# Performance work log

Measured on AMD Instinct MI355X. Metric: run time of the kernel, lower is better.

Reference implementation:

```python
import jax, jax.numpy as jnp
import numpy as np

ROPE_THETA = 10000.0

def _apply_rope(x, theta=ROPE_THETA):
    # x: [B, H, L, d_head]
    L, d_k = x.shape[-2], x.shape[-1]
    inv_freq = 1.0 / (theta ** (jnp.arange(0, d_k, 2, dtype=jnp.float32) / d_k))  # [d_k/2]
    ang = jnp.arange(L, dtype=jnp.float32)[:, None] * inv_freq[None, :]           # [L, d_k/2]
    ang = jnp.repeat(ang, 2, axis=-1)                                             # [L, d_k] interleaved
    xr = x.reshape(x.shape[:-1] + (d_k // 2, 2))
    rot = jnp.stack((-xr[..., 1], xr[..., 0]), axis=-1).reshape(x.shape)
    return x * jnp.cos(ang) + rot * jnp.sin(ang)

def setup_inputs() -> dict:
    key = jax.random.key(0)
    k1, k2, k3 = jax.random.split(key, 3)
    B, L, D = 2, 2048, 2048
    std_qkv = np.sqrt(2.0 / (D + 3 * D)).astype(np.float32)
    std_o = np.sqrt(2.0 / (D + D)).astype(np.float32)
    return {
        "x": jax.random.normal(k1, (B, L, D), dtype=jnp.float32),
        "W_qkv": jax.random.normal(k2, (3 * D, D), dtype=jnp.float32) * std_qkv,
        "W_o": jax.random.normal(k3, (D, D), dtype=jnp.float32) * std_o,
    }

def reference(x, W_qkv, W_o):
    B, L, D = x.shape
    H = 16
    dh = D // H
    qkv = jnp.einsum('bld,ed->ble', x, W_qkv)            # [B, L, 3D]
    q, k, v = jnp.split(qkv, 3, axis=-1)
    # [B, H, L, dh]
    q = q.reshape(B, L, H, dh).transpose(0, 2, 1, 3)
    k = k.reshape(B, L, H, dh).transpose(0, 2, 1, 3)
    v = v.reshape(B, L, H, dh).transpose(0, 2, 1, 3)
    q = _apply_rope(q)
    k = _apply_rope(k)
    scale = 1.0 / np.sqrt(dh).astype(np.float32)
    att = jnp.einsum('bhqd,bhkd->bhqk', q, k) * scale    # [B, H, L, L]
    causal = jnp.tril(jnp.ones((L, L), dtype=bool))
    att = jnp.where(causal, att, -jnp.inf)
    p = jax.nn.softmax(att, axis=-1)
    y = jnp.einsum('bhqk,bhkd->bhqd', p, v)              # [B, H, L, dh]
    y = y.transpose(0, 2, 1, 3).reshape(B, L, D)
    return jnp.einsum('bld,ed->ble', y, W_o)
```

## Files before the change

### kernel.cpp

```cpp
#include <hip/hip_runtime.h>
#include <math.h>

typedef __bf16 bf16x8 __attribute__((ext_vector_type(8)));
typedef float f32x4 __attribute__((ext_vector_type(4)));
typedef unsigned short us8 __attribute__((ext_vector_type(8)));

#define B_ 2
#define L_ 2048
#define D_ 2048
#define H_ 16
#define DH 128

__device__ __forceinline__ unsigned short f2b(float f) {
  union { float f; unsigned u; } v; v.f = f;
  unsigned u = v.u;
  return (unsigned short)((u + 0x7fffu + ((u >> 16) & 1u)) >> 16);
}
__device__ __forceinline__ float b2f(unsigned short h) {
  union { unsigned u; float f; } v; v.u = ((unsigned)h) << 16;
  return v.f;
}

#define GLD16(g, l) __builtin_amdgcn_global_load_lds(                          \
    (const __attribute__((address_space(1))) void*)(g),                        \
    (__attribute__((address_space(3))) void*)(l), 16, 0, 0)

__global__ void f32_to_bf16(const float* __restrict__ in,
                            unsigned short* __restrict__ out, int n4) {
  int i = blockIdx.x * blockDim.x + threadIdx.x;
  const int stride = gridDim.x * blockDim.x;
  for (; i < n4; i += stride) {
    const float4 v = ((const float4*)in)[i];
    ushort4 o;
    o.x = f2b(v.x); o.y = f2b(v.y); o.z = f2b(v.z); o.w = f2b(v.w);
    ((ushort4*)out)[i] = o;
  }
}


#define SB()                              \
  do {                                    \
    __builtin_amdgcn_s_barrier();         \
    __builtin_amdgcn_sched_barrier(0);    \
  } while (0)

#define VMC2() asm volatile("s_waitcnt vmcnt(2)" ::: "memory")

#define LOAD_A(BUF, MH)                                                        \
  _Pragma("unroll") for (int q = 0; q < 4; ++q) {                              \
    const int rowA = (MH) * 64 + q * 16 + lo;                                  \
    _Pragma("unroll") for (int kk = 0; kk < 2; ++kk)                           \
        af[q][kk] = *(const bf16x8*)&lds[0][BUF][wmh]                          \
            [rowA * 64 + ((kk * 4 + hi) ^ sw) * 8];                            \
  }

#define LOAD_B(BUF, NH)                                                        \
  _Pragma("unroll") for (int j = 0; j < 2; ++j) {                              \
    const int rowB = bro + ((NH) * 2 + j) * 16;                                \
    _Pragma("unroll") for (int kk = 0; kk < 2; ++kk)                           \
        bfr[j][kk] = *(const bf16x8*)&lds[1][BUF][bhalf]                       \
            [rowB * 64 + ((kk * 4 + hi) ^ sw) * 8];                            \
  }

#define MFMA16(MH, NH)                                                         \
  do {                                                                         \
    __builtin_amdgcn_s_setprio(1);                                             \
    _Pragma("unroll") for (int q = 0; q < 4; ++q) {                            \
      _Pragma("unroll") for (int j = 0; j < 2; ++j) {                          \
        acc[(MH) * 4 + q][(NH) * 2 + j] =                                      \
            __builtin_amdgcn_mfma_f32_16x16x32_bf16(                           \
                af[q][0], bfr[j][0], acc[(MH) * 4 + q][(NH) * 2 + j], 0, 0, 0);\
        acc[(MH) * 4 + q][(NH) * 2 + j] =                                      \
            __builtin_amdgcn_mfma_f32_16x16x32_bf16(                           \
                af[q][1], bfr[j][1], acc[(MH) * 4 + q][(NH) * 2 + j], 0, 0, 0);\
      }                                                                        \
    }                                                                          \
    __builtin_amdgcn_s_setprio(0);                                             \
  } while (0)

template <bool OUT_BF16>
__global__ __launch_bounds__(512)
void gemm8p(const unsigned short* __restrict__ A,
            const unsigned short* __restrict__ Bm,
            void* __restrict__ Cv, int M, int N, int K) {
  __shared__ __align__(16) unsigned short lds[2][2][2][128 * 64];
  const int tid = threadIdx.x;
  const int w = tid >> 6, lane = tid & 63;
  const int lo = lane & 15, hi = lane >> 4, sw = lo & 7;
  const int wmh = w >> 2;
  const int wn = (w & 3) * 64;
  const int bhalf = wn >> 7, bro = (wn & 64) + lo;
  const int GM = M >> 8;
  const int nwg = gridDim.x;
  const int f = blockIdx.x;
  const int v = (f & 7) * (nwg >> 3) + (f >> 3);
  const int bn = v / GM, bm = v % GM;
  const int NI = K >> 7;

  auto stageU = [&](int mat, int buf, int half, int tile) {
    const unsigned short* G = mat ? Bm : A;
    const int r256 = (mat ? bn : bm) * 256 + half * 128;
#pragma unroll
    for (int u = 0; u < 2; ++u) {
      const int c = u * 512 + tid;
      const int row = c >> 3;
      const int gs = (c & 7) ^ (row & 7);
      GLD16(G + (long)(r256 + row) * K + tile * 64 + gs * 8,
            &lds[mat][buf][half][(u * 512 + (tid & ~63)) * 8]);
    }
  };

  f32x4 acc[8][4] = {};
  bf16x8 af[4][2], bfr[2][2];

  stageU(0, 0, 0, 0); stageU(0, 0, 1, 0);
  stageU(1, 0, 0, 0); stageU(1, 0, 1, 0);
  stageU(0, 1, 0, 1);
  VMC2();
  SB();

  for (int i = 0; i < NI; ++i) {
    const int t1 = 2 * i + 1;
    const bool nx = (i + 1 < NI);
    LOAD_A(0, 0) LOAD_B(0, 0)
    stageU(1, 1, 0, t1);
    SB(); MFMA16(0, 0); SB();
    LOAD_B(0, 1)
    stageU(0, 1, 1, t1);
    SB(); MFMA16(0, 1); SB();
    LOAD_A(0, 1)
    stageU(1, 1, 1, t1);
    SB(); MFMA16(1, 1); SB();
    LOAD_B(0, 0)
    if (nx) stageU(0, 0, 0, t1 + 1);
    SB(); MFMA16(1, 0);
    VMC2();
    SB();
    LOAD_A(1, 0) LOAD_B(1, 0)
    if (nx) stageU(0, 0, 1, t1 + 1);
    SB(); MFMA16(0, 0); SB();
    LOAD_B(1, 1)
    if (nx) stageU(1, 0, 0, t1 + 1);
    SB(); MFMA16(0, 1); SB();
    LOAD_A(1, 1)
    if (nx) stageU(1, 0, 1, t1 + 1);
    SB(); MFMA16(1, 1); SB();
    LOAD_B(1, 0)
    if (nx) stageU(0, 1, 0, t1 + 2);
    SB(); MFMA16(1, 0);
    VMC2();
    SB();
  }

  const int r0 = bm * 256 + wmh * 128;
  const int c0 = bn * 256 + wn;
#pragma unroll
  for (int mi = 0; mi < 8; ++mi) {
#pragma unroll
    for (int r = 0; r < 4; ++r) {
      const long row = r0 + mi * 16 + hi * 4 + r;
#pragma unroll
      for (int ni = 0; ni < 4; ++ni) {
        const int col = c0 + ni * 16 + lo;
        if (OUT_BF16)
          ((unsigned short*)Cv)[row * N + col] = f2b(acc[mi][ni][r]);
        else
          ((float*)Cv)[row * N + col] = acc[mi][ni][r];
      }
    }
  }
}

__global__ void rope_qk(const unsigned short* __restrict__ qkv,
                        unsigned short* __restrict__ Qo,
                        unsigned short* __restrict__ Ko) {
  const int idx = blockIdx.x * 256 + threadIdx.x;
  const int i = idx & 63;
  const int l = (idx >> 6) & (L_ - 1);
  const int h = (idx >> 17) & (H_ - 1);
  const int b = idx >> 21;
  const float invf = exp2f(-(float)i * 0.20762050593045077f);
  const float ang = (float)l * invf;
  float sn, cs;
  sincosf(ang, &sn, &cs);
  const long base = ((long)b * L_ + l) * (3 * D_) + h * DH + 2 * i;
  const unsigned qin = *(const unsigned*)&qkv[base];
  const unsigned kin = *(const unsigned*)&qkv[base + D_];
  const float q0 = b2f((unsigned short)qin), q1 = b2f((unsigned short)(qin >> 16));
  const float k0 = b2f((unsigned short)kin), k1 = b2f((unsigned short)(kin >> 16));
  const float sc = 0.12751743f;
  const float qo0 = (q0 * cs - q1 * sn) * sc, qo1 = (q1 * cs + q0 * sn) * sc;
  const float ko0 = (k0 * cs - k1 * sn), ko1 = (k1 * cs + k0 * sn);
  const long oo = ((long)(b * H_ + h) * L_ + l) * DH + 2 * i;
  *(unsigned*)&Qo[oo] = (unsigned)f2b(qo0) | ((unsigned)f2b(qo1) << 16);
  *(unsigned*)&Ko[oo] = (unsigned)f2b(ko0) | ((unsigned)f2b(ko1) << 16);
}

__global__ __launch_bounds__(256)
void v_fragpack(const unsigned short* __restrict__ qkv,
                unsigned short* __restrict__ Vf) {
  const int lblk = blockIdx.x;
  const int bh = blockIdx.y;
  const int b = bh >> 4, h = bh & 15;
  __shared__ unsigned short tile[64 * 137];
  const int tid = threadIdx.x;
  const int l0 = lblk * 64;
#pragma unroll
  for (int j = 0; j < 4; ++j) {
    const int c = j * 256 + tid;
    const int row = c >> 4, col8 = c & 15;
    const us8 v = *(const us8*)&qkv[((long)b * L_ + l0 + row) * (3 * D_) +
                                    2 * D_ + h * DH + col8 * 8];
    unsigned short* dst = &tile[row * 137 + col8 * 8];
#pragma unroll
    for (int e = 0; e < 8; ++e) dst[e] = v[e];
  }
  __syncthreads();
#pragma unroll
  for (int j = 0; j < 4; ++j) {
    const int c = j * 256 + tid;
    const int k32l = c >> 9, t2 = (c >> 6) & 7, lane = c & 63;
    const int lo = lane & 15, hi = lane >> 4;
    us8 v;
#pragma unroll
    for (int e = 0; e < 8; ++e)
      v[e] = tile[(k32l * 32 + hi * 8 + e) * 137 + t2 * 16 + lo];
    *(us8*)&Vf[(((size_t)bh * 64 + lblk * 2 + k32l) * 8 + t2) * 512 + lane * 8] = v;
  }
}

__global__ __launch_bounds__(256, 2)
void flash_attn3(const unsigned short* __restrict__ Q,
                 const unsigned short* __restrict__ Kg,
                 const unsigned short* __restrict__ Vf,
                 unsigned short* __restrict__ Y) {
  const int p = blockIdx.x;
  const int tA = p, tB = (L_ / 64 - 1) - p;
  const int h = blockIdx.y, b = blockIdx.z;
  const int tid = threadIdx.x;
  const int wave = tid >> 6, lane = tid & 63;
  const int lo = lane & 15, hi = lane >> 4;
  const int swz = (lo & 7) << 4;
  const int qA = tA * 64 + wave * 16;
  const int qB = tB * 64 + wave * 16;
  const long hoff = ((long)(b * H_ + h)) * L_ * DH;
  const unsigned short* Qh = Q + hoff;
  const unsigned short* Kh = Kg + hoff;
  const unsigned short* Vfh = Vf + ((size_t)(b * H_ + h)) * (64 * 8 * 512);

  __shared__ unsigned short lK[2][64 * 128];
  __shared__ unsigned short pl[4][2][16 * 72];
  unsigned short* plA = &pl[wave][0][0];
  unsigned short* plB = &pl[wave][1][0];

  auto stage = [&](int bufi, int kv0s) {
    unsigned short* bk = &lK[bufi][0];
#pragma unroll
    for (int j = 0; j < 4; ++j) {
      const int c = j * 256 + tid;
      const int row = c >> 4;
      const int soff = ((c & 15) ^ (row & 7)) << 3;
      GLD16(Kh + (long)(kv0s + row) * DH + soff, &bk[(c & ~63) * 8]);
    }
  };

  bf16x8 qfA[4], qfB[4];
#pragma unroll
  for (int s = 0; s < 4; ++s) {
    qfA[s] = *(const bf16x8*)&Qh[(long)(qA + lo) * DH + s * 32 + hi * 8];
    qfB[s] = *(const bf16x8*)&Qh[(long)(qB + lo) * DH + s * 32 + hi * 8];
  }

  float mA = -INFINITY, lsA = 0.f, mB = -INFINITY, lsB = 0.f;
  f32x4 yA[8] = {}, yB[8] = {};

  auto softmax = [&](f32x4 (&st)[4], float& m, float& lsum, f32x4 (&yacc)[8],
                     unsigned short* plw, int qw, int kv0) {
    if (kv0 + 63 > qw) {
      const int d0 = qw + lo - kv0 - hi * 4;
#pragma unroll
      for (int t = 0; t < 4; ++t) {
        const int dt = d0 - t * 16;
#pragma unroll
        for (int r = 0; r < 4; ++r)
          if (r > dt) st[t][r] = -INFINITY;
      }
    }
    float tm0 = fmaxf(fmaxf(st[0][0], st[0][1]), fmaxf(st[0][2], st[0][3]));
    float tm1 = fmaxf(fmaxf(st[1][0], st[1][1]), fmaxf(st[1][2], st[1][3]));
    float tm2 = fmaxf(fmaxf(st[2][0], st[2][1]), fmaxf(st[2][2], st[2][3]));
    float tm3 = fmaxf(fmaxf(st[3][0], st[3][1]), fmaxf(st[3][2], st[3][3]));
    float rm = fmaxf(fmaxf(tm0, tm1), fmaxf(tm2, tm3));
    rm = fmaxf(rm, __shfl_xor(rm, 16));
    rm = fmaxf(rm, __shfl_xor(rm, 32));
    if (!__all(rm <= m + 8.f)) {
      const float mn = fmaxf(m, rm);
      const float alpha = exp2f(m - mn);
      m = mn;
      lsum *= alpha;
      float ar[4];
#pragma unroll
      for (int r = 0; r < 4; ++r) ar[r] = __shfl(alpha, hi * 4 + r);
#pragma unroll
      for (int t2 = 0; t2 < 8; ++t2)
#pragma unroll
        for (int r = 0; r < 4; ++r) yacc[t2][r] *= ar[r];
    }
    float rs = 0.f;
#pragma unroll
    for (int t = 0; t < 4; ++t) {
#pragma unroll
      for (int r2 = 0; r2 < 2; ++r2) {
        const float e0 = exp2f(st[t][2 * r2] - m);
        const float e1 = exp2f(st[t][2 * r2 + 1] - m);
        rs += e0 + e1;
        const unsigned short u0 = __builtin_bit_cast(unsigned short, (__bf16)e0);
        const unsigned short u1 = __builtin_bit_cast(unsigned short, (__bf16)e1);
        *(unsigned*)&plw[lo * 72 + t * 16 + hi * 4 + 2 * r2] =
            (unsigned)u0 | ((unsigned)u1 << 16);
      }
    }
    rs += __shfl_xor(rs, 16);
    rs += __shfl_xor(rs, 32);
    lsum += rs;
  };

  const int nIter = tB + 1;
  stage(0, 0);
  __syncthreads();

  for (int it = 0; it < nIter; ++it) {
    const int kv0 = it * 64;
    const bool aAct = (it <= tA);
    if (it + 1 < nIter) stage((it + 1) & 1, kv0 + 64);
    const char* bkc = (const char*)&lK[it & 1][0];
    f32x4 stA[4] = {}, stB[4] = {};
    if (aAct) {
#pragma unroll
      for (int s = 0; s < 4; ++s) {
        const int inner = (lo * 256 + s * 64 + hi * 16) ^ swz;
#pragma unroll
        for (int t = 0; t < 4; ++t) {
          const bf16x8 kf = *(const bf16x8*)(bkc + t * 4096 + inner);
          stA[t] = __builtin_amdgcn_mfma_f32_16x16x32_bf16(kf, qfA[s], stA[t], 0, 0, 0);
          stB[t] = __builtin_amdgcn_mfma_f32_16x16x32_bf16(kf, qfB[s], stB[t], 0, 0, 0);
        }
      }
    } else {
#pragma unroll
      for (int s = 0; s < 4; ++s) {
        const int inner = (lo * 256 + s * 64 + hi * 16) ^ swz;
#pragma unroll
        for (int t = 0; t < 4; ++t) {
          const bf16x8 kf = *(const bf16x8*)(bkc + t * 4096 + inner);
          stB[t] = __builtin_amdgcn_mfma_f32_16x16x32_bf16(kf, qfB[s], stB[t], 0, 0, 0);
        }
      }
    }
    if (aAct) softmax(stA, mA, lsA, yA, plA, qA, kv0);
    softmax(stB, mB, lsB, yB, plB, qB, kv0);
    const unsigned short* vbase = Vfh + (size_t)(it * 16) * 512 + lane * 8;
#pragma unroll
    for (int kt = 0; kt < 2; ++kt) {
      bf16x8 vf[8];
#pragma unroll
      for (int t2 = 0; t2 < 8; ++t2)
        vf[t2] = *(const bf16x8*)(vbase + (size_t)(kt * 8 + t2) * 512);
      const bf16x8 pfB = *(const bf16x8*)&plB[lo * 72 + kt * 32 + hi * 8];
#pragma unroll
      for (int t2 = 0; t2 < 8; ++t2)
        yB[t2] = __builtin_amdgcn_mfma_f32_16x16x32_bf16(pfB, vf[t2], yB[t2], 0, 0, 0);
      if (aAct) {
        const bf16x8 pfA = *(const bf16x8*)&plA[lo * 72 + kt * 32 + hi * 8];
#pragma unroll
        for (int t2 = 0; t2 < 8; ++t2)
          yA[t2] = __builtin_amdgcn_mfma_f32_16x16x32_bf16(pfA, vf[t2], yA[t2], 0, 0, 0);
      }
    }
    __syncthreads();
  }

  auto wout = [&](f32x4 (&yacc)[8], float lsum, int qw) {
    const float inv = 1.f / lsum;
    float ir[4];
#pragma unroll
    for (int r = 0; r < 4; ++r) ir[r] = __shfl(inv, hi * 4 + r);
#pragma unroll
    for (int r = 0; r < 4; ++r) {
      const long row = qw + hi * 4 + r;
      unsigned short* yrow = Y + ((long)b * L_ + row) * D_ + h * DH;
#pragma unroll
      for (int t2 = 0; t2 < 8; ++t2)
        yrow[t2 * 16 + lo] = f2b(yacc[t2][r] * ir[r]);
    }
  };
  wout(yA, lsA, qA);
  wout(yB, lsB, qB);
}

extern "C" void kernel_launch(void* const* d_in, const int* in_sizes, int n_in,
                              void* d_out, int out_size, void* d_ws, size_t ws_size,
                              hipStream_t stream) {
  const float* x = (const float*)d_in[0];
  const float* wqkv = (const float*)d_in[1];
  const float* wo = (const float*)d_in[2];
  float* out = (float*)d_out;

  unsigned short* ws = (unsigned short*)d_ws;
  const size_t N_X = (size_t)B_ * L_ * D_;
  const size_t N_WQKV = (size_t)3 * D_ * D_;
  const size_t N_WO = (size_t)D_ * D_;
  const size_t N_QKV = (size_t)B_ * L_ * 3 * D_;
  const size_t N_HEAD = (size_t)B_ * H_ * L_ * DH;
  unsigned short* xb = ws;
  unsigned short* wqkb = xb + N_X;
  unsigned short* wob = wqkb + N_WQKV;
  unsigned short* qkv = wob + N_WO;
  unsigned short* Qb = qkv + N_QKV;
  unsigned short* Kb = Qb + N_HEAD;
  unsigned short* Vf = Kb + N_HEAD;
  unsigned short* Yb = Vf + N_HEAD;
  const size_t need = (size_t)(Yb + N_HEAD - ws) * sizeof(unsigned short);
  if (ws_size < need) return;

  f32_to_bf16<<<2048, 256, 0, stream>>>(x, xb, (int)(N_X / 4));
  f32_to_bf16<<<2048, 256, 0, stream>>>(wqkv, wqkb, (int)(N_WQKV / 4));
  f32_to_bf16<<<2048, 256, 0, stream>>>(wo, wob, (int)(N_WO / 4));

  gemm8p<true><<<(B_ * L_ / 256) * (3 * D_ / 256), 512, 0, stream>>>(
      xb, wqkb, qkv, B_ * L_, 3 * D_, D_);

  rope_qk<<<(B_ * H_ * L_ * 64) / 256, 256, 0, stream>>>(qkv, Qb, Kb);
  v_fragpack<<<dim3(L_ / 64, B_ * H_), 256, 0, stream>>>(qkv, Vf);

  flash_attn3<<<dim3(16, H_, B_), 256, 0, stream>>>(Qb, Kb, Vf, Yb);

  gemm8p<false><<<(B_ * L_ / 256) * (D_ / 256), 512, 0, stream>>>(
      Yb, wob, out, B_ * L_, D_, D_);
}
```

Before: 296.4 us.

## Keep both B fragment halves in registers and restage GEMM loads in pairs

The B operand fragments are now held for both N halves (bfr[NH]), so the fourth MFMA phase of each half-iteration reuses registers instead of reloading B from LDS. Global-to-LDS staging is regrouped so that both halves of a matrix tile are issued together, and the wait count changes to vmcnt(4), with vmcnt(0) on the last iteration. This cuts LDS reads and changes how global loads overlap with compute. The cost is more VGPRs at 512-thread launch bounds, plus a different prefetch depth that could expose load latency.

```diff
diff --git a/kernel.cpp b/kernel.cpp
--- a/kernel.cpp
+++ b/kernel.cpp
@@ -44,7 +44,8 @@
     __builtin_amdgcn_sched_barrier(0);    \
   } while (0)
 
-#define VMC2() asm volatile("s_waitcnt vmcnt(2)" ::: "memory")
+#define VMC4() asm volatile("s_waitcnt vmcnt(4)" ::: "memory")
+#define VMC0() asm volatile("s_waitcnt vmcnt(0)" ::: "memory")
 
 #define LOAD_A(BUF, MH)                                                        \
   _Pragma("unroll") for (int q = 0; q < 4; ++q) {                              \
@@ -58,7 +59,7 @@
   _Pragma("unroll") for (int j = 0; j < 2; ++j) {                              \
     const int rowB = bro + ((NH) * 2 + j) * 16;                                \
     _Pragma("unroll") for (int kk = 0; kk < 2; ++kk)                           \
-        bfr[j][kk] = *(const bf16x8*)&lds[1][BUF][bhalf]                       \
+        bfr[NH][j][kk] = *(const bf16x8*)&lds[1][BUF][bhalf]                   \
             [rowB * 64 + ((kk * 4 + hi) ^ sw) * 8];                            \
   }
 
@@ -69,10 +70,12 @@
       _Pragma("unroll") for (int j = 0; j < 2; ++j) {                          \
         acc[(MH) * 4 + q][(NH) * 2 + j] =                                      \
             __builtin_amdgcn_mfma_f32_16x16x32_bf16(                           \
-                af[q][0], bfr[j][0], acc[(MH) * 4 + q][(NH) * 2 + j], 0, 0, 0);\
+                af[q][0], bfr[NH][j][0], acc[(MH) * 4 + q][(NH) * 2 + j],      \
+                0, 0, 0);                                                      \
         acc[(MH) * 4 + q][(NH) * 2 + j] =                                      \
             __builtin_amdgcn_mfma_f32_16x16x32_bf16(                           \
-                af[q][1], bfr[j][1], acc[(MH) * 4 + q][(NH) * 2 + j], 0, 0, 0);\
+                af[q][1], bfr[NH][j][1], acc[(MH) * 4 + q][(NH) * 2 + j],      \
+                0, 0, 0);                                                      \
       }                                                                        \
     }                                                                          \
     __builtin_amdgcn_s_setprio(0);                                             \
@@ -111,44 +114,38 @@
   };
 
   f32x4 acc[8][4] = {};
-  bf16x8 af[4][2], bfr[2][2];
+  bf16x8 af[4][2], bfr[2][2][2];
 
   stageU(0, 0, 0, 0); stageU(0, 0, 1, 0);
   stageU(1, 0, 0, 0); stageU(1, 0, 1, 0);
-  stageU(0, 1, 0, 1);
-  VMC2();
+  stageU(0, 1, 0, 1); stageU(0, 1, 1, 1);
+  VMC4();
   SB();
 
   for (int i = 0; i < NI; ++i) {
-    const int t1 = 2 * i + 1;
+    const int tOdd = 2 * i + 1;
     const bool nx = (i + 1 < NI);
     LOAD_A(0, 0) LOAD_B(0, 0)
-    stageU(1, 1, 0, t1);
+    stageU(1, 1, 0, tOdd); stageU(1, 1, 1, tOdd);
     SB(); MFMA16(0, 0); SB();
     LOAD_B(0, 1)
-    stageU(0, 1, 1, t1);
     SB(); MFMA16(0, 1); SB();
     LOAD_A(0, 1)
-    stageU(1, 1, 1, t1);
     SB(); MFMA16(1, 1); SB();
-    LOAD_B(0, 0)
-    if (nx) stageU(0, 0, 0, t1 + 1);
+    if (nx) { stageU(0, 0, 0, tOdd + 1); stageU(0, 0, 1, tOdd + 1); }
     SB(); MFMA16(1, 0);
-    VMC2();
+    if (nx) VMC4(); else VMC0();
     SB();
     LOAD_A(1, 0) LOAD_B(1, 0)
-    if (nx) stageU(0, 0, 1, t1 + 1);
+    if (nx) { stageU(1, 0, 0, tOdd + 1); stageU(1, 0, 1, tOdd + 1); }
     SB(); MFMA16(0, 0); SB();
     LOAD_B(1, 1)
-    if (nx) stageU(1, 0, 0, t1 + 1);
     SB(); MFMA16(0, 1); SB();
     LOAD_A(1, 1)
-    if (nx) stageU(1, 0, 1, t1 + 1);
     SB(); MFMA16(1, 1); SB();
-    LOAD_B(1, 0)
-    if (nx) stageU(0, 1, 0, t1 + 2);
+    if (nx) { stageU(0, 1, 0, tOdd + 2); stageU(0, 1, 1, tOdd + 2); }
     SB(); MFMA16(1, 0);
-    VMC2();
+    if (nx) VMC4(); else VMC0();
     SB();
   }
 
```

Result: slower. 304.0 us (+2.6%).
